# Kernel tuning notes

Hardware: AMD Instinct MI355X
Metric: run time of the kernel (lower is better)

## Reference

```python
import jax, jax.numpy as jnp
import numpy as np

B, S, DIM = 1, 2048, 2048
NH, NKV, HD = 32, 8, 64
NREP = NH // NKV  # 4


def setup_inputs() -> dict:
    key = jax.random.key(0)
    ks = jax.random.split(key, 5)
    x = jax.random.normal(ks[0], (B, S, DIM), jnp.float32)
    # torch nn.Linear weight layout: (out_features, in_features)
    wq = jax.random.normal(ks[1], (NH * HD, DIM), jnp.float32) * (DIM ** -0.5)
    wk = jax.random.normal(ks[2], (NKV * HD, DIM), jnp.float32) * (DIM ** -0.5)
    wv = jax.random.normal(ks[3], (NKV * HD, DIM), jnp.float32) * (DIM ** -0.5)
    wo = jax.random.normal(ks[4], (DIM, NH * HD), jnp.float32) * ((NH * HD) ** -0.5)
    # Llama-style rotary frequencies: angle[t, i] = t / 10000^(2i/head_dim)
    inv_freq = 1.0 / (10000.0 ** (np.arange(0, HD, 2, dtype=np.float64) / HD))  # (HD/2,)
    ang = np.outer(np.arange(S, dtype=np.float64), inv_freq)                     # (S, HD/2)
    freqs_cis = jnp.asarray(np.stack([np.cos(ang), np.sin(ang)], axis=-1), jnp.float32)  # (S, HD/2, 2)
    # additive causal mask, shape (1, 1, S, S)
    mask = jnp.triu(jnp.full((S, S), -1e9, jnp.float32), k=1)[None, None]
    return dict(x=x, wq=wq, wk=wk, wv=wv, wo=wo, freqs_cis=freqs_cis, mask=mask)


def _apply_rope(x, cos, sin):
    # x: (B, S, H, HD); rotate adjacent pairs along last dim
    xr = x.reshape(x.shape[:-1] + (-1, 2))
    x1, x2 = xr[..., 0], xr[..., 1]
    c = cos[None, :, None, :]  # (1, S, 1, HD/2)
    s = sin[None, :, None, :]
    out = jnp.stack([x1 * c - x2 * s, x1 * s + x2 * c], axis=-1)
    return out.reshape(x.shape)


def reference(x, wq, wk, wv, wo, freqs_cis, mask):
    b, s, _ = x.shape
    q = (x @ wq.T).reshape(b, s, NH, HD)
    k = (x @ wk.T).reshape(b, s, NKV, HD)
    v = (x @ wv.T).reshape(b, s, NKV, HD)
    cos, sin = freqs_cis[..., 0], freqs_cis[..., 1]
    q = _apply_rope(q, cos, sin)
    k = _apply_rope(k, cos, sin)
    # GQA: group q heads by kv head instead of materializing repeated K/V
    qg = q.reshape(b, s, NKV, NREP, HD)
    scale = HD ** -0.5
    # scores: (b, g=kv_head, r=rep, s=q_pos, t=k_pos)
    scores = jnp.einsum('bsgrd,btgd->bgrst', qg, k) * scale
    scores = scores + mask[:, :, None]  # (1,1,1,S,S) broadcast
    p = jax.nn.softmax(scores.astype(jnp.float32), axis=-1).astype(q.dtype)
    out = jnp.einsum('bgrst,btgd->bsgrd', p, v).reshape(b, s, NH * HD)
    return out @ wo.T
```

## Files before the change

### kernel.cpp

```cpp
#include <hip/hip_runtime.h>
#include <hip/hip_bf16.h>

#define S_LEN 2048
#define DIM_  2048
#define NH    32
#define NKV   8
#define HD    64

typedef __bf16 bf16x8 __attribute__((ext_vector_type(8)));
typedef __bf16 bf16x4 __attribute__((ext_vector_type(4)));
typedef float  f32x4  __attribute__((ext_vector_type(4)));

#define AS_GLOBAL(p) ((const __attribute__((address_space(1))) void*)(p))
#define AS_LDS(p)    ((__attribute__((address_space(3))) void*)(p))

__global__ __launch_bounds__(256) void cvt_xw(
    const float* __restrict__ x,  const float* __restrict__ wq,
    const float* __restrict__ wk, const float* __restrict__ wv,
    const float* __restrict__ wo,
    __bf16* __restrict__ xb, __bf16* __restrict__ wb, __bf16* __restrict__ wob)
{
  size_t i = (size_t)blockIdx.x * 256 + threadIdx.x;
  const float* src; __bf16* dst; size_t off;
  if (i < 1048576)      { src = x;  dst = xb;            off = i; }
  else if (i < 2097152) { src = wq; dst = wb;            off = i - 1048576; }
  else if (i < 2359296) { src = wk; dst = wb + 4194304;  off = i - 2097152; }
  else if (i < 2621440) { src = wv; dst = wb + 5242880;  off = i - 2359296; }
  else                  { src = wo; dst = wob;           off = i - 2621440; }
  float4 f = ((const float4*)src)[off];
  bf16x4 r;
  r[0] = (__bf16)f.x; r[1] = (__bf16)f.y; r[2] = (__bf16)f.z; r[3] = (__bf16)f.w;
  ((bf16x4*)dst)[off] = r;
}

#define BK 32
#define TA_ELEMS 4096
#define TB_ELEMS 2048

__device__ __forceinline__ void stage_A(
    const __bf16* __restrict__ g, int row0, int k0, int ld, __bf16* lds)
{
  const int tid = threadIdx.x;
  const int wave = tid >> 6;
#pragma unroll
  for (int iss = 0; iss < 2; ++iss) {
    int off = (iss * 256 + tid) * 16;
    int r = off >> 6;
    int c = (off & 63) >> 1;
    __builtin_amdgcn_global_load_lds(
        AS_GLOBAL(g + (size_t)(row0 + r) * ld + k0 + c),
        AS_LDS(lds + iss * 2048 + wave * 512),
        16, 0, 0);
  }
}

__device__ __forceinline__ void stage_B(
    const __bf16* __restrict__ g, int row0, int k0, int ld, __bf16* lds)
{
  const int tid = threadIdx.x;
  int off = tid * 16;
  int r = off >> 6;
  int c = (off & 63) >> 1;
  __builtin_amdgcn_global_load_lds(
      AS_GLOBAL(g + (size_t)(row0 + r) * ld + k0 + c),
      AS_LDS(lds + (tid >> 6) * 512), 16, 0, 0);
}

__device__ __forceinline__ void gemm_mainloop(
    const __bf16* __restrict__ A, const __bf16* __restrict__ B,
    int row0, int col0, int lda, int ldb, int nt,
    __bf16* As, __bf16* Bs, f32x4 acc[4][2])
{
  const int lane = threadIdx.x & 63;
  const int wave = threadIdx.x >> 6;
  const int wr = wave >> 1, wc = wave & 1;
  const int fr = lane & 15, fg = lane >> 4;

  stage_A(A, row0, 0, lda, As);
  stage_B(B, col0, 0, ldb, Bs);

  for (int t = 0; t < nt; ++t) {
    const int cur = t & 1;
    if (t + 1 < nt) {
      stage_A(A, row0, (t + 1) * BK, lda, As + (cur ^ 1) * TA_ELEMS);
      stage_B(B, col0, (t + 1) * BK, ldb, Bs + (cur ^ 1) * TB_ELEMS);
    }
    __syncthreads();
    bf16x8 a[4], b[2];
#pragma unroll
    for (int mi = 0; mi < 4; ++mi)
      a[mi] = *(const bf16x8*)(As + cur * TA_ELEMS + (wr * 64 + mi * 16 + fr) * 32 + fg * 8);
#pragma unroll
    for (int ni = 0; ni < 2; ++ni)
      b[ni] = *(const bf16x8*)(Bs + cur * TB_ELEMS + (wc * 32 + ni * 16 + fr) * 32 + fg * 8);
#pragma unroll
    for (int mi = 0; mi < 4; ++mi)
#pragma unroll
      for (int ni = 0; ni < 2; ++ni)
        acc[mi][ni] = __builtin_amdgcn_mfma_f32_16x16x32_bf16(a[mi], b[ni], acc[mi][ni], 0, 0, 0);
    __syncthreads();
  }
}

__global__ __launch_bounds__(256) void qkv_gemm(
    const __bf16* __restrict__ xb, const __bf16* __restrict__ wb,
    __bf16* __restrict__ q_buf, __bf16* __restrict__ k_buf, __bf16* __restrict__ v_buf)
{
  __shared__ __bf16 As[2 * TA_ELEMS];
  __shared__ __bf16 Bs[2 * TB_ELEMS];
  const int lane = threadIdx.x & 63;
  const int wave = threadIdx.x >> 6;
  const int wr = wave >> 1, wc = wave & 1;
  const int fr = lane & 15, fg = lane >> 4;

  const int lid = blockIdx.x;
  const int xcd = lid & 7;
  const int i   = lid >> 3;
  const int row0 = (i & 15) * 128;
  const int col0 = (xcd * 6 + (i >> 4)) * 64;

  f32x4 acc[4][2] = {};
  gemm_mainloop(xb, wb, row0, col0, DIM_, DIM_, DIM_ / BK, As, Bs, acc);

  const int rowg0 = row0 + wr * 64;
  const int colg0 = col0 + wc * 32;
#pragma unroll
  for (int mi = 0; mi < 4; ++mi) {
#pragma unroll
    for (int ni = 0; ni < 2; ++ni) {
#pragma unroll
      for (int j = 0; j < 4; ++j) {
        int row = rowg0 + mi * 16 + fg * 4 + j;
        int col = colg0 + ni * 16 + fr;
        float v = acc[mi][ni][j];
        if (col < 2048) {
          int h = col >> 6, d = col & 63;
          q_buf[((size_t)h * S_LEN + row) * HD + d] = (__bf16)v;
        } else if (col < 2560) {
          int c = col - 2048, g = c >> 6, d = c & 63;
          k_buf[((size_t)g * S_LEN + row) * HD + d] = (__bf16)v;
        } else {
          int c = col - 2560, g = c >> 6, d = c & 63;
          v_buf[((size_t)g * HD + d) * S_LEN + row] = (__bf16)v;
        }
      }
    }
  }
}

__global__ __launch_bounds__(256) void oproj_gemm(
    const __bf16* __restrict__ attn_buf, const __bf16* __restrict__ wob,
    float* __restrict__ out)
{
  __shared__ __bf16 As[2 * TA_ELEMS];
  __shared__ __bf16 Bs[2 * TB_ELEMS];
  const int lane = threadIdx.x & 63;
  const int wave = threadIdx.x >> 6;
  const int wr = wave >> 1, wc = wave & 1;
  const int fr = lane & 15, fg = lane >> 4;

  const int lid = blockIdx.x;
  const int xcd = lid & 7;
  const int i   = lid >> 3;
  const int row0 = (i & 15) * 128;
  const int col0 = (xcd * 4 + (i >> 4)) * 64;

  f32x4 acc[4][2] = {};
  gemm_mainloop(attn_buf, wob, row0, col0, DIM_, DIM_, DIM_ / BK, As, Bs, acc);

  const int rowg0 = row0 + wr * 64;
  const int colg0 = col0 + wc * 32;
#pragma unroll
  for (int mi = 0; mi < 4; ++mi)
#pragma unroll
    for (int ni = 0; ni < 2; ++ni)
#pragma unroll
      for (int j = 0; j < 4; ++j) {
        int row = rowg0 + mi * 16 + fg * 4 + j;
        int col = colg0 + ni * 16 + fr;
        out[(size_t)row * DIM_ + col] = acc[mi][ni][j];
      }
}

__global__ __launch_bounds__(256) void rope_k(
    __bf16* __restrict__ k_buf, const float* __restrict__ fc)
{
  int idx = blockIdx.x * 256 + threadIdx.x;
  int i    = idx & 31;
  int sp   = (idx >> 5) & (S_LEN - 1);
  int g    = idx >> 16;
  __bf16* buf = k_buf + ((size_t)g * S_LEN + sp) * HD;
  float c = fc[(sp * 32 + i) * 2 + 0];
  float s = fc[(sp * 32 + i) * 2 + 1];
  float x1 = (float)buf[2 * i], x2 = (float)buf[2 * i + 1];
  buf[2 * i + 0] = (__bf16)(x1 * c - x2 * s);
  buf[2 * i + 1] = (__bf16)(x1 * s + x2 * c);
}

__global__ __launch_bounds__(512) void attn_kernel(
    const __bf16* __restrict__ q_buf, const __bf16* __restrict__ k_buf,
    const __bf16* __restrict__ v_buf, const float* __restrict__ fc,
    __bf16* __restrict__ attn_buf)
{
  __shared__ __align__(16) __bf16 Ks[2][64 * 64];
  __shared__ __align__(16) __bf16 Vs[2][64 * 64];
  __shared__ __align__(16) __bf16 lds_p[8][16][72];

  const int tid  = threadIdx.x;
  const int lane = tid & 63;
  const int wave = tid >> 6;
  const int n = blockIdx.x;
  const int qt = (n < 256) ? (15 - (n >> 5)) : ((n - 256) >> 5);
  const int h  = n & 31;
  const int g = h >> 2;
  const int r0 = qt * 128 + wave * 16;
  const int lrow = lane & 15;
  const int lgrp = lane >> 4;
  const int lk = lgrp * 8;

  const __bf16* qh = q_buf + (size_t)h * S_LEN * HD;
  const __bf16* kh = k_buf + (size_t)g * S_LEN * HD;
  const __bf16* vh = v_buf + (size_t)g * HD * S_LEN;

  const int sr   = tid >> 3;
  const int scol = tid & 7;
  const int dcol = scol ^ (sr & 7);

  bf16x8 qa[2];
  const float* fcrow = fc + (size_t)(r0 + lrow) * 64;
#pragma unroll
  for (int kk = 0; kk < 2; ++kk) {
    qa[kk] = *(const bf16x8*)(qh + (size_t)(r0 + lrow) * HD + kk * 32 + lk);
    float4 cs0 = *(const float4*)(fcrow + (kk * 16 + lgrp * 4) * 2);
    float4 cs1 = *(const float4*)(fcrow + (kk * 16 + lgrp * 4) * 2 + 4);
    float cc[4] = {cs0.x, cs0.z, cs1.x, cs1.z};
    float ss[4] = {cs0.y, cs0.w, cs1.y, cs1.w};
#pragma unroll
    for (int pr = 0; pr < 4; ++pr) {
      float x1 = (float)qa[kk][2 * pr], x2 = (float)qa[kk][2 * pr + 1];
      qa[kk][2 * pr]     = (__bf16)(x1 * cc[pr] - x2 * ss[pr]);
      qa[kk][2 * pr + 1] = (__bf16)(x1 * ss[pr] + x2 * cc[pr]);
    }
  }

  const float KS = 0.125f * 1.44269504088896f;
  float m_col = -3.0e38f, l_col = 0.f;
  f32x4 oacc[4] = {};

  const int nt = 2 * qt + 2;

  {
    uint4 k0 = *(const uint4*)(kh + (size_t)sr * HD + scol * 8);
    uint4 v0 = *(const uint4*)(vh + (size_t)sr * S_LEN + scol * 8);
    *(uint4*)(&Ks[0][sr * 64 + dcol * 8]) = k0;
    *(uint4*)(&Vs[0][sr * 64 + dcol * 8]) = v0;
  }
  __syncthreads();

  for (int t = 0; t < nt; ++t) {
    const int cur = t & 1;
    const int t0 = t * 64;

    const int tn0 = (t + 1 < nt ? t + 1 : t) * 64;
    uint4 kreg = *(const uint4*)(kh + (size_t)(tn0 + sr) * HD + scol * 8);
    uint4 vreg = *(const uint4*)(vh + (size_t)sr * S_LEN + tn0 + scol * 8);

    const int dmax = r0 + 15 - t0;
    if (dmax >= 0) {
      f32x4 sc[4] = {};
      const int cmax = dmax >> 4;
      __builtin_amdgcn_s_setprio(1);
#pragma unroll
      for (int c = 0; c < 4; ++c) {
        if (c <= cmax) {
#pragma unroll
          for (int kk = 0; kk < 2; ++kk) {
            bf16x8 ka = *(const bf16x8*)(
                &Ks[cur][(c * 16 + lrow) * 64 + (((kk * 4 + lgrp) ^ (lrow & 7)) * 8)]);
            sc[c] = __builtin_amdgcn_mfma_f32_16x16x32_bf16(ka, qa[kk], sc[c], 0, 0, 0);
          }
        }
      }
      __builtin_amdgcn_s_setprio(0);

      float p[16];
      const int q = r0 + lrow;
      if (t0 + 63 <= r0) {
#pragma unroll
        for (int c = 0; c < 4; ++c)
#pragma unroll
          for (int j = 0; j < 4; ++j)
            p[c * 4 + j] = sc[c][j] * KS;
      } else {
#pragma unroll
        for (int c = 0; c < 4; ++c)
#pragma unroll
          for (int j = 0; j < 4; ++j) {
            int kv = t0 + c * 16 + lgrp * 4 + j;
            p[c * 4 + j] = (kv <= q) ? sc[c][j] * KS : -3.0e38f;
          }
      }

      float m8[8], m4[4];
#pragma unroll
      for (int i = 0; i < 8; ++i) m8[i] = fmaxf(p[i], p[i + 8]);
#pragma unroll
      for (int i = 0; i < 4; ++i) m4[i] = fmaxf(m8[i], m8[i + 4]);
      float mx = fmaxf(fmaxf(m4[0], m4[1]), fmaxf(m4[2], m4[3]));
      mx = fmaxf(mx, __shfl_xor(mx, 16, 64));
      mx = fmaxf(mx, __shfl_xor(mx, 32, 64));

      if (__all(mx <= m_col + 8.f)) {
      } else {
        float nm = fmaxf(m_col, mx);
        float alpha = __builtin_amdgcn_exp2f(m_col - nm);
        m_col = nm;
        float ar[4];
#pragma unroll
        for (int j = 0; j < 4; ++j)
          ar[j] = __shfl(alpha, lgrp * 4 + j, 64);
#pragma unroll
        for (int nf = 0; nf < 4; ++nf)
#pragma unroll
          for (int j = 0; j < 4; ++j)
            oacc[nf][j] *= ar[j];
        l_col *= alpha;
      }

#pragma unroll
      for (int i = 0; i < 16; ++i)
        p[i] = __builtin_amdgcn_exp2f(p[i] - m_col);
      float s8[8], s4[4];
#pragma unroll
      for (int i = 0; i < 8; ++i) s8[i] = p[i] + p[i + 8];
#pragma unroll
      for (int i = 0; i < 4; ++i) s4[i] = s8[i] + s8[i + 4];
      float rs = (s4[0] + s4[1]) + (s4[2] + s4[3]);
      rs += __shfl_xor(rs, 16, 64);
      rs += __shfl_xor(rs, 32, 64);
      l_col += rs;

#pragma unroll
      for (int c = 0; c < 4; ++c)
#pragma unroll
        for (int e = 0; e < 2; ++e) {
          union { __bf16 hh[2]; unsigned u; } pk;
          pk.hh[0] = (__bf16)p[c * 4 + 2 * e];
          pk.hh[1] = (__bf16)p[c * 4 + 2 * e + 1];
          *(unsigned*)&lds_p[wave][lrow][c * 16 + lgrp * 4 + 2 * e] = pk.u;
        }
      asm volatile("s_waitcnt lgkmcnt(0)" ::: "memory");

      bf16x8 pa0 = *(const bf16x8*)&lds_p[wave][lrow][lk];
      __builtin_amdgcn_s_setprio(1);
#pragma unroll
      for (int nf = 0; nf < 4; ++nf) {
        bf16x8 vb = *(const bf16x8*)(
            &Vs[cur][(nf * 16 + lrow) * 64 + ((lgrp ^ (lrow & 7)) * 8)]);
        oacc[nf] = __builtin_amdgcn_mfma_f32_16x16x32_bf16(pa0, vb, oacc[nf], 0, 0, 0);
      }
      __builtin_amdgcn_s_setprio(0);
      if (dmax >= 32) {
        bf16x8 pa1 = *(const bf16x8*)&lds_p[wave][lrow][32 + lk];
        __builtin_amdgcn_s_setprio(1);
#pragma unroll
        for (int nf = 0; nf < 4; ++nf) {
          bf16x8 vb = *(const bf16x8*)(
              &Vs[cur][(nf * 16 + lrow) * 64 + (((4 + lgrp) ^ (lrow & 7)) * 8)]);
          oacc[nf] = __builtin_amdgcn_mfma_f32_16x16x32_bf16(pa1, vb, oacc[nf], 0, 0, 0);
        }
        __builtin_amdgcn_s_setprio(0);
      }
    }

    *(uint4*)(&Ks[cur ^ 1][sr * 64 + dcol * 8]) = kreg;
    *(uint4*)(&Vs[cur ^ 1][sr * 64 + dcol * 8]) = vreg;
    __syncthreads();
  }

  float rlr[4];
#pragma unroll
  for (int j = 0; j < 4; ++j)
    rlr[j] = 1.0f / __shfl(l_col, lgrp * 4 + j, 64);
#pragma unroll
  for (int nf = 0; nf < 4; ++nf)
#pragma unroll
    for (int j = 0; j < 4; ++j) {
      int row = r0 + lgrp * 4 + j;
      attn_buf[(size_t)row * (NH * HD) + h * HD + nf * 16 + lrow] =
          (__bf16)(oacc[nf][j] * rlr[j]);
    }
}

extern "C" void kernel_launch(void* const* d_in, const int* in_sizes, int n_in,
                              void* d_out, int out_size, void* d_ws, size_t ws_size,
                              hipStream_t stream)
{
  const float* x  = (const float*)d_in[0];
  const float* wq = (const float*)d_in[1];
  const float* wk = (const float*)d_in[2];
  const float* wv = (const float*)d_in[3];
  const float* wo = (const float*)d_in[4];
  const float* fc = (const float*)d_in[5];
  float* out = (float*)d_out;

  char* ws = (char*)d_ws;
  __bf16* q_buf    = (__bf16*)(ws);
  __bf16* k_buf    = (__bf16*)(ws +  8u * 1024 * 1024);
  __bf16* v_buf    = (__bf16*)(ws + 10u * 1024 * 1024);
  __bf16* attn_buf = (__bf16*)(ws + 12u * 1024 * 1024);
  __bf16* xb       = (__bf16*)(ws + 20u * 1024 * 1024);
  __bf16* wb       = (__bf16*)(ws + 28u * 1024 * 1024);
  __bf16* wob      = (__bf16*)(ws + 40u * 1024 * 1024);

  cvt_xw<<<dim3(14336), 256, 0, stream>>>(x, wq, wk, wv, wo, xb, wb, wob);
  qkv_gemm<<<dim3(768), 256, 0, stream>>>(xb, wb, q_buf, k_buf, v_buf);
  rope_k<<<dim3(2048), 256, 0, stream>>>(k_buf, fc);
  attn_kernel<<<dim3(512), 512, 0, stream>>>(q_buf, k_buf, v_buf, fc, attn_buf);
  oproj_gemm<<<dim3(512), 256, 0, stream>>>(attn_buf, wob, out);
}
```

Before: 150.4 us.

## Enlarge GEMM tiles to 128x128 and use three-stage LDS prefetch pipeline

The QKV and output-projection GEMMs now use 128x128 block tiles, with each wave computing a 64x64 sub-tile, which halves the launched grids. Staging moves from two-buffer double buffering with two block barriers per step to a three-buffer ring that prefetches two tiles ahead, with one barrier and a partial vmcnt wait. This aims to raise operand reuse per LDS load and hide global latency better. In exchange it uses more registers and LDS per block, and the smaller grids may leave CUs idle or create tail imbalance.

```diff
diff --git a/kernel.cpp b/kernel.cpp
--- a/kernel.cpp
+++ b/kernel.cpp
@@ -33,14 +33,13 @@
   ((bf16x4*)dst)[off] = r;
 }
 
-#define BK 32
-#define TA_ELEMS 4096
-#define TB_ELEMS 2048
-
-__device__ __forceinline__ void stage_A(
+#define BKG   32
+#define TILEG 4096
+
+__device__ __forceinline__ void stageG(
     const __bf16* __restrict__ g, int row0, int k0, int ld, __bf16* lds)
 {
-  const int tid = threadIdx.x;
+  const int tid  = threadIdx.x;
   const int wave = tid >> 6;
 #pragma unroll
   for (int iss = 0; iss < 2; ++iss) {
@@ -54,51 +53,48 @@
   }
 }
 
-__device__ __forceinline__ void stage_B(
-    const __bf16* __restrict__ g, int row0, int k0, int ld, __bf16* lds)
-{
-  const int tid = threadIdx.x;
-  int off = tid * 16;
-  int r = off >> 6;
-  int c = (off & 63) >> 1;
-  __builtin_amdgcn_global_load_lds(
-      AS_GLOBAL(g + (size_t)(row0 + r) * ld + k0 + c),
-      AS_LDS(lds + (tid >> 6) * 512), 16, 0, 0);
-}
-
-__device__ __forceinline__ void gemm_mainloop(
+__device__ __forceinline__ void gemm_pipe(
     const __bf16* __restrict__ A, const __bf16* __restrict__ B,
-    int row0, int col0, int lda, int ldb, int nt,
-    __bf16* As, __bf16* Bs, f32x4 acc[4][2])
+    int row0, int col0, int ld, int nt,
+    __bf16* As, __bf16* Bs, f32x4 acc[4][4])
 {
   const int lane = threadIdx.x & 63;
   const int wave = threadIdx.x >> 6;
   const int wr = wave >> 1, wc = wave & 1;
   const int fr = lane & 15, fg = lane >> 4;
 
-  stage_A(A, row0, 0, lda, As);
-  stage_B(B, col0, 0, ldb, Bs);
-
+  stageG(A, row0, 0, ld, As);
+  stageG(B, col0, 0, ld, Bs);
+  stageG(A, row0, BKG, ld, As + TILEG);
+  stageG(B, col0, BKG, ld, Bs + TILEG);
+
+  int cur = 0, pb = 2;
   for (int t = 0; t < nt; ++t) {
-    const int cur = t & 1;
-    if (t + 1 < nt) {
-      stage_A(A, row0, (t + 1) * BK, lda, As + (cur ^ 1) * TA_ELEMS);
-      stage_B(B, col0, (t + 1) * BK, ldb, Bs + (cur ^ 1) * TB_ELEMS);
-    }
-    __syncthreads();
-    bf16x8 a[4], b[2];
+    asm volatile("" ::: "memory");
+    __builtin_amdgcn_s_barrier();
+    asm volatile("" ::: "memory");
+
+    const int tn = (t + 2 < nt) ? t + 2 : nt - 1;
+    stageG(A, row0, tn * BKG, ld, As + pb * TILEG);
+    stageG(B, col0, tn * BKG, ld, Bs + pb * TILEG);
+
+    asm volatile("s_waitcnt vmcnt(8)" ::: "memory");
+
+    bf16x8 a[4], b[4];
 #pragma unroll
     for (int mi = 0; mi < 4; ++mi)
-      a[mi] = *(const bf16x8*)(As + cur * TA_ELEMS + (wr * 64 + mi * 16 + fr) * 32 + fg * 8);
-#pragma unroll
-    for (int ni = 0; ni < 2; ++ni)
-      b[ni] = *(const bf16x8*)(Bs + cur * TB_ELEMS + (wc * 32 + ni * 16 + fr) * 32 + fg * 8);
+      a[mi] = *(const bf16x8*)(As + cur * TILEG + (wr * 64 + mi * 16 + fr) * 32 + fg * 8);
+#pragma unroll
+    for (int ni = 0; ni < 4; ++ni)
+      b[ni] = *(const bf16x8*)(Bs + cur * TILEG + (wc * 64 + ni * 16 + fr) * 32 + fg * 8);
 #pragma unroll
     for (int mi = 0; mi < 4; ++mi)
 #pragma unroll
-      for (int ni = 0; ni < 2; ++ni)
+      for (int ni = 0; ni < 4; ++ni)
         acc[mi][ni] = __builtin_amdgcn_mfma_f32_16x16x32_bf16(a[mi], b[ni], acc[mi][ni], 0, 0, 0);
-    __syncthreads();
+
+    cur = (cur == 2) ? 0 : cur + 1;
+    pb  = (pb  == 2) ? 0 : pb  + 1;
   }
 }
 
@@ -106,8 +102,8 @@
     const __bf16* __restrict__ xb, const __bf16* __restrict__ wb,
     __bf16* __restrict__ q_buf, __bf16* __restrict__ k_buf, __bf16* __restrict__ v_buf)
 {
-  __shared__ __bf16 As[2 * TA_ELEMS];
-  __shared__ __bf16 Bs[2 * TB_ELEMS];
+  __shared__ __bf16 As[3 * TILEG];
+  __shared__ __bf16 Bs[3 * TILEG];
   const int lane = threadIdx.x & 63;
   const int wave = threadIdx.x >> 6;
   const int wr = wave >> 1, wc = wave & 1;
@@ -115,24 +111,24 @@
 
   const int lid = blockIdx.x;
   const int xcd = lid & 7;
-  const int i   = lid >> 3;
-  const int row0 = (i & 15) * 128;
-  const int col0 = (xcd * 6 + (i >> 4)) * 64;
-
-  f32x4 acc[4][2] = {};
-  gemm_mainloop(xb, wb, row0, col0, DIM_, DIM_, DIM_ / BK, As, Bs, acc);
+  const int j   = lid >> 3;
+  const int col0 = (xcd * 3 + (j >> 4)) * 128;
+  const int row0 = (j & 15) * 128;
+
+  f32x4 acc[4][4] = {};
+  gemm_pipe(xb, wb, row0, col0, DIM_, DIM_ / BKG, As, Bs, acc);
 
   const int rowg0 = row0 + wr * 64;
-  const int colg0 = col0 + wc * 32;
+  const int colg0 = col0 + wc * 64;
 #pragma unroll
   for (int mi = 0; mi < 4; ++mi) {
 #pragma unroll
-    for (int ni = 0; ni < 2; ++ni) {
-#pragma unroll
-      for (int j = 0; j < 4; ++j) {
-        int row = rowg0 + mi * 16 + fg * 4 + j;
+    for (int ni = 0; ni < 4; ++ni) {
+#pragma unroll
+      for (int j2 = 0; j2 < 4; ++j2) {
+        int row = rowg0 + mi * 16 + fg * 4 + j2;
         int col = colg0 + ni * 16 + fr;
-        float v = acc[mi][ni][j];
+        float v = acc[mi][ni][j2];
         if (col < 2048) {
           int h = col >> 6, d = col & 63;
           q_buf[((size_t)h * S_LEN + row) * HD + d] = (__bf16)v;
@@ -152,8 +148,8 @@
     const __bf16* __restrict__ attn_buf, const __bf16* __restrict__ wob,
     float* __restrict__ out)
 {
-  __shared__ __bf16 As[2 * TA_ELEMS];
-  __shared__ __bf16 Bs[2 * TB_ELEMS];
+  __shared__ __bf16 As[3 * TILEG];
+  __shared__ __bf16 Bs[3 * TILEG];
   const int lane = threadIdx.x & 63;
   const int wave = threadIdx.x >> 6;
   const int wr = wave >> 1, wc = wave & 1;
@@ -161,24 +157,24 @@
 
   const int lid = blockIdx.x;
   const int xcd = lid & 7;
-  const int i   = lid >> 3;
-  const int row0 = (i & 15) * 128;
-  const int col0 = (xcd * 4 + (i >> 4)) * 64;
-
-  f32x4 acc[4][2] = {};
-  gemm_mainloop(attn_buf, wob, row0, col0, DIM_, DIM_, DIM_ / BK, As, Bs, acc);
+  const int j   = lid >> 3;
+  const int col0 = (xcd * 2 + (j >> 4)) * 128;
+  const int row0 = (j & 15) * 128;
+
+  f32x4 acc[4][4] = {};
+  gemm_pipe(attn_buf, wob, row0, col0, DIM_, DIM_ / BKG, As, Bs, acc);
 
   const int rowg0 = row0 + wr * 64;
-  const int colg0 = col0 + wc * 32;
+  const int colg0 = col0 + wc * 64;
 #pragma unroll
   for (int mi = 0; mi < 4; ++mi)
 #pragma unroll
-    for (int ni = 0; ni < 2; ++ni)
-#pragma unroll
-      for (int j = 0; j < 4; ++j) {
-        int row = rowg0 + mi * 16 + fg * 4 + j;
+    for (int ni = 0; ni < 4; ++ni)
+#pragma unroll
+      for (int j2 = 0; j2 < 4; ++j2) {
+        int row = rowg0 + mi * 16 + fg * 4 + j2;
         int col = colg0 + ni * 16 + fr;
-        out[(size_t)row * DIM_ + col] = acc[mi][ni][j];
+        out[(size_t)row * DIM_ + col] = acc[mi][ni][j2];
       }
 }
 
@@ -414,8 +410,8 @@
   __bf16* wob      = (__bf16*)(ws + 40u * 1024 * 1024);
 
   cvt_xw<<<dim3(14336), 256, 0, stream>>>(x, wq, wk, wv, wo, xb, wb, wob);
-  qkv_gemm<<<dim3(768), 256, 0, stream>>>(xb, wb, q_buf, k_buf, v_buf);
+  qkv_gemm<<<dim3(384), 256, 0, stream>>>(xb, wb, q_buf, k_buf, v_buf);
   rope_k<<<dim3(2048), 256, 0, stream>>>(k_buf, fc);
   attn_kernel<<<dim3(512), 512, 0, stream>>>(q_buf, k_buf, v_buf, fc, attn_buf);
-  oproj_gemm<<<dim3(512), 256, 0, stream>>>(attn_buf, wob, out);
-}
+  oproj_gemm<<<dim3(256), 256, 0, stream>>>(attn_buf, wob, out);
+}
```

Result: slower. 157.3 us (+4.6%).
